# Kernel optimization log

Hardware: AMD Instinct MI355X
Metric: run time of the kernel (lower is better)

## Reference

```python
import jax, jax.numpy as jnp
import numpy as np


def setup_inputs() -> dict:
    key = jax.random.key(0)
    ks = jax.random.split(key, 4)
    B, H, W, C = 4, 64, 64, 256
    d = C // 8
    x = jax.random.normal(ks[0], (B, H, W, C), dtype=jnp.float32)
    wq = jax.random.normal(ks[1], (C, d), dtype=jnp.float32) * (1.0 / np.sqrt(C))
    wk = jax.random.normal(ks[2], (C, d), dtype=jnp.float32) * (1.0 / np.sqrt(C))
    wv = jax.random.normal(ks[3], (C, C), dtype=jnp.float32) * (1.0 / np.sqrt(C))
    bq = jnp.zeros((d,), dtype=jnp.float32)
    bk = jnp.zeros((d,), dtype=jnp.float32)
    bv = jnp.zeros((C,), dtype=jnp.float32)
    return {"x": x, "wq": wq, "bq": bq, "wk": wk, "bk": bk, "wv": wv, "bv": bv}


def reference(x, wq, bq, wk, bk, wv, bv):
    # x: [B, H, W, C] (channels-last, as in Keras Conv2D default)
    B, H, W, C = x.shape
    N = H * W
    xf = x.reshape(B, N, C)                      # 1x1 conv == per-pixel matmul
    q = xf @ wq + bq                             # [B, N, C//8]
    k = xf @ wk + bk                             # [B, N, C//8]
    v = xf @ wv + bv                             # [B, N, C]
    # NOTE: original module applies NO 1/sqrt(d) scaling.
    attn = jax.nn.softmax(jnp.einsum('bnd,bmd->bnm', q, k), axis=-1)  # [B, N, N]
    out = jnp.einsum('bnm,bmc->bnc', attn, v)    # [B, N, C]
    return out.reshape(B, H, W, C) + x
```

## Files before the change

### kernel.cpp

```cpp
#include <hip/hip_runtime.h>
#include <stdint.h>

typedef _Float16 f16;
typedef f16 half8 __attribute__((ext_vector_type(8)));
typedef f16 half4 __attribute__((ext_vector_type(4)));
typedef float floatx4 __attribute__((ext_vector_type(4)));

#define MFMA_F16(A, B, Cc) __builtin_amdgcn_mfma_f32_16x16x32_f16((A), (B), (Cc), 0, 0, 0)

static constexpr int NB  = 4;
static constexpr int NN  = 4096;
static constexpr int NC  = 256;
static constexpr int ND  = 32;
static constexpr int PIX = NB * NN;
static constexpr int NS  = 4;
static constexpr int KS  = NN / NS;

__device__ f16 g_WbT[320 * 256];
__device__ f16 g_Qh[(size_t)PIX * ND];
__device__ f16 g_Kh[(size_t)PIX * ND];
__device__ f16 g_VbT[(size_t)NB * NC * NN];
__device__ f16 g_Of[(size_t)NS * PIX * NC];
__device__ float g_m[NS * PIX];
__device__ float g_l[NS * PIX];

__device__ inline void gl2lds16(const f16* g, f16* l) {
  __builtin_amdgcn_global_load_lds(
      (const __attribute__((address_space(1))) void*)g,
      (__attribute__((address_space(3))) void*)l, 16, 0, 0);
}

__global__ __launch_bounds__(256) void prep_weights(const float* __restrict__ wq,
                                                    const float* __restrict__ wk,
                                                    const float* __restrict__ wv) {
  const int tid = blockIdx.x * 256 + threadIdx.x;
  if (tid >= 320 * 256) return;
  const int j = tid >> 8;
  const int k = tid & 255;
  float v;
  if (j < 32)      v = wq[k * 32 + j];
  else if (j < 64) v = wk[k * 32 + (j - 32)];
  else             v = wv[k * 256 + (j - 64)];
  g_WbT[j * 256 + k] = (f16)v;
}

__global__ __launch_bounds__(256) void proj_qkv(const float* __restrict__ x,
                                                const float* __restrict__ bq,
                                                const float* __restrict__ bk,
                                                const float* __restrict__ bv) {
  __shared__ f16 xs[64 * 32];
  __shared__ f16 wsT[320 * 32];
  __shared__ f16 vt[256 * 64];

  const int tid  = threadIdx.x;
  const int lane = tid & 63;
  const int wid  = tid >> 6;
  const int qd   = lane >> 4;
  const int c16  = lane & 15;
  const int p0   = blockIdx.x * 64;
  const floatx4 zero4 = {0.f, 0.f, 0.f, 0.f};

  floatx4 acc[20];
#pragma unroll
  for (int i = 0; i < 20; ++i) acc[i] = zero4;

  for (int kk = 0; kk < 256; kk += 32) {
    {
      const int r = tid >> 2, g = tid & 3;
      const floatx4* s4 = (const floatx4*)(x + (size_t)(p0 + r) * NC + kk + g * 8);
      const floatx4 xa = s4[0], xb = s4[1];
      half8 h;
      h[0] = (f16)xa[0]; h[1] = (f16)xa[1]; h[2] = (f16)xa[2]; h[3] = (f16)xa[3];
      h[4] = (f16)xb[0]; h[5] = (f16)xb[1]; h[6] = (f16)xb[2]; h[7] = (f16)xb[3];
      *(half8*)&xs[r * 32 + g * 8] = h;
    }
#pragma unroll
    for (int i = 0; i < 10; ++i) {
      const int cid = tid + 256 * i;
      const int j = cid >> 3, m = cid & 7;
      *(half4*)&wsT[j * 32 + m * 4] = *(const half4*)&g_WbT[j * 256 + kk + m * 4];
    }
    __syncthreads();
    const half8 a = *(const half8*)&xs[(wid * 16 + c16) * 32 + qd * 8];
#pragma unroll
    for (int nt = 0; nt < 20; ++nt) {
      const half8 bfr = *(const half8*)&wsT[(nt * 16 + c16) * 32 + qd * 8];
      acc[nt] = MFMA_F16(a, bfr, acc[nt]);
    }
    __syncthreads();
  }

#pragma unroll
  for (int nt = 0; nt < 20; ++nt) {
    const int j = nt * 16 + c16;
    const float bias = (j < 32) ? bq[j] : (j < 64) ? bk[j - 32] : bv[j - 64];
#pragma unroll
    for (int r = 0; r < 4; ++r) {
      const int rl = wid * 16 + qd * 4 + r;
      const int p  = p0 + rl;
      const float val = acc[nt][r] + bias;
      if (j < 32) {
        g_Qh[(size_t)p * ND + j] = (f16)(val * 1.44269504f);
      } else if (j < 64) {
        g_Kh[(size_t)p * ND + (j - 32)] = (f16)val;
      } else {
        vt[(j - 64) * 64 + rl] = (f16)val;
      }
    }
  }
  __syncthreads();
  const int b  = p0 >> 12;
  const int n0 = p0 & (NN - 1);
#pragma unroll
  for (int i = 0; i < 16; ++i) {
    const int cid = tid + 256 * i;
    const int c = cid >> 4, m = cid & 15;
    *(half4*)(g_VbT + ((size_t)(b * NC + c)) * NN + n0 + m * 4) =
        *(const half4*)&vt[c * 64 + m * 4];
  }
}

__global__ __launch_bounds__(256, 2) void attn_split(void) {
  __shared__ f16 vsT[256 * 64];
  __shared__ f16 ps[4][2][16 * 64];

  const int tid  = threadIdx.x;
  const int lane = tid & 63;
  const int wid  = tid >> 6;
  const int qd   = lane >> 4;
  const int c16  = lane & 15;
  const int b    = blockIdx.y;
  const int s    = blockIdx.z;
  const int q0   = blockIdx.x * 128 + wid * 32;
  const int sx7  = c16 & 7;
  const floatx4 zero4 = {0.f, 0.f, 0.f, 0.f};

  const int vrow = wid * 64 + (lane >> 3);
  const int vchk = (lane & 7) ^ ((lane >> 3) & 7);
  const f16* vlane = g_VbT + ((size_t)(b * NC + vrow)) * NN + vchk * 8;
  f16* vdst = &vsT[(size_t)wid * 4096 + (size_t)0];

  half8 qf[2];
#pragma unroll
  for (int g = 0; g < 2; ++g)
    qf[g] = *(const half8*)(g_Qh + ((size_t)(b * NN + q0 + g * 16 + c16)) * ND + qd * 8);

  floatx4 acc[2][16];
#pragma unroll
  for (int g = 0; g < 2; ++g)
#pragma unroll
    for (int i = 0; i < 16; ++i) acc[g][i] = zero4;
  float m_i[2] = {-1e30f, -1e30f};
  float l_p[2] = {0.f, 0.f};

  const int kbeg = s * KS, kend = (s + 1) * KS;

#pragma unroll
  for (int i = 0; i < 8; ++i)
    gl2lds16(vlane + kbeg + i * 8 * NN, vdst + i * 512);
  half8 kreg[4];
#pragma unroll
  for (int a = 0; a < 4; ++a)
    kreg[a] = *(const half8*)(g_Kh + ((size_t)(b * NN + kbeg + a * 16 + c16)) * ND + qd * 8);

  for (int k0 = kbeg; k0 < kend; k0 += 64) {
    floatx4 st[2][4];
#pragma unroll
    for (int g = 0; g < 2; ++g)
#pragma unroll
      for (int a = 0; a < 4; ++a) st[g][a] = MFMA_F16(kreg[a], qf[g], zero4);

    float tm[2];
#pragma unroll
    for (int g = 0; g < 2; ++g) {
      float t0 = fmaxf(fmaxf(st[g][0][0], st[g][0][1]), fmaxf(st[g][0][2], st[g][0][3]));
      float t1 = fmaxf(fmaxf(st[g][1][0], st[g][1][1]), fmaxf(st[g][1][2], st[g][1][3]));
      float t2 = fmaxf(fmaxf(st[g][2][0], st[g][2][1]), fmaxf(st[g][2][2], st[g][2][3]));
      float t3 = fmaxf(fmaxf(st[g][3][0], st[g][3][1]), fmaxf(st[g][3][2], st[g][3][3]));
      tm[g] = fmaxf(fmaxf(t0, t1), fmaxf(t2, t3));
    }
    if (__any(tm[0] > m_i[0] || tm[1] > m_i[1])) {
#pragma unroll
      for (int g = 0; g < 2; ++g) {
        float tr = tm[g];
        tr = fmaxf(tr, __shfl_xor(tr, 16));
        tr = fmaxf(tr, __shfl_xor(tr, 32));
        const float m_new = (tr > m_i[g]) ? tr + 5.0f : m_i[g];
        const float alpha = exp2f(m_i[g] - m_new);
        m_i[g] = m_new;
        l_p[g] *= alpha;
        float a4[4];
#pragma unroll
        for (int r = 0; r < 4; ++r) a4[r] = __shfl(alpha, qd * 4 + r);
#pragma unroll
        for (int ct = 0; ct < 16; ++ct)
#pragma unroll
          for (int r = 0; r < 4; ++r) acc[g][ct][r] *= a4[r];
      }
    }

#pragma unroll
    for (int g = 0; g < 2; ++g) {
      float ts = 0.f;
#pragma unroll
      for (int a = 0; a < 4; ++a) {
        half4 h;
#pragma unroll
        for (int r = 0; r < 4; ++r) {
          const float p = exp2f(st[g][a][r] - m_i[g]);
          ts += p;
          h[r] = (f16)p;
        }
        const int pc = ((a * 2 + (qd >> 1)) ^ sx7) * 8 + (qd & 1) * 4;
        *(half4*)&ps[wid][g][c16 * 64 + pc] = h;
      }
      l_p[g] += ts;
    }

    __syncthreads();

    const int k0n = (k0 + 64 < kend) ? (k0 + 64) : kbeg;
    half8 knew[4];
#pragma unroll
    for (int a = 0; a < 4; ++a)
      knew[a] = *(const half8*)(g_Kh + ((size_t)(b * NN + k0n + a * 16 + c16)) * ND + qd * 8);

    half8 pa[2][2];
#pragma unroll
    for (int g = 0; g < 2; ++g)
#pragma unroll
      for (int kh = 0; kh < 2; ++kh)
        pa[g][kh] = *(const half8*)&ps[wid][g][c16 * 64 + ((kh * 4 + qd) ^ sx7) * 8];
#pragma unroll
    for (int ct = 0; ct < 16; ++ct) {
#pragma unroll
      for (int kh = 0; kh < 2; ++kh) {
        const half8 bfr =
            *(const half8*)&vsT[(ct * 16 + c16) * 64 + ((kh * 4 + qd) ^ sx7) * 8];
        acc[0][ct] = MFMA_F16(pa[0][kh], bfr, acc[0][ct]);
        acc[1][ct] = MFMA_F16(pa[1][kh], bfr, acc[1][ct]);
      }
    }
    __syncthreads();

    if (k0 + 64 < kend) {
#pragma unroll
      for (int i = 0; i < 8; ++i)
        gl2lds16(vlane + (k0 + 64) + i * 8 * NN, vdst + i * 512);
    }
#pragma unroll
    for (int a = 0; a < 4; ++a) kreg[a] = knew[a];
  }

#pragma unroll
  for (int g = 0; g < 2; ++g) {
    float l = l_p[g];
    l += __shfl_xor(l, 16);
    l += __shfl_xor(l, 32);
    if (qd == 0) {
      const int row = b * NN + q0 + g * 16 + c16;
      g_m[s * PIX + row] = m_i[g];
      g_l[s * PIX + row] = l;
    }
    float linv[4];
#pragma unroll
    for (int r = 0; r < 4; ++r) linv[r] = 1.0f / __shfl(l, qd * 4 + r);
#pragma unroll
    for (int ct = 0; ct < 16; ++ct)
#pragma unroll
      for (int r = 0; r < 4; ++r) {
        const int qrow = q0 + g * 16 + qd * 4 + r;
        const int c = ct * 16 + c16;
        g_Of[((size_t)(s * PIX + b * NN + qrow)) * NC + c] = (f16)(acc[g][ct][r] * linv[r]);
      }
  }
}

__global__ __launch_bounds__(256) void combine(const float* __restrict__ x,
                                               float* __restrict__ out) {
  const int tid  = threadIdx.x;
  const int lane = tid & 63;
  const int wid  = tid >> 6;
  const int row  = blockIdx.x * 4 + wid;
  const int c    = lane * 4;

  float m[NS], l[NS], M = -1e30f;
#pragma unroll
  for (int s = 0; s < NS; ++s) {
    m[s] = g_m[s * PIX + row];
    l[s] = g_l[s * PIX + row];
    M = fmaxf(M, m[s]);
  }
  float w[NS], den = 0.f;
#pragma unroll
  for (int s = 0; s < NS; ++s) { w[s] = l[s] * exp2f(m[s] - M); den += w[s]; }
  const float inv = 1.0f / den;

  float a0 = 0.f, a1 = 0.f, a2 = 0.f, a3 = 0.f;
#pragma unroll
  for (int s = 0; s < NS; ++s) {
    const half4 h = *(const half4*)&g_Of[((size_t)(s * PIX + row)) * NC + c];
    const float ws = w[s] * inv;
    a0 += ws * (float)h[0];
    a1 += ws * (float)h[1];
    a2 += ws * (float)h[2];
    a3 += ws * (float)h[3];
  }
  const floatx4 xv = *(const floatx4*)&x[(size_t)row * NC + c];
  floatx4 o;
  o[0] = a0 + xv[0]; o[1] = a1 + xv[1]; o[2] = a2 + xv[2]; o[3] = a3 + xv[3];
  *(floatx4*)&out[(size_t)row * NC + c] = o;
}

extern "C" void kernel_launch(void* const* d_in, const int* in_sizes, int n_in,
                              void* d_out, int out_size, void* d_ws, size_t ws_size,
                              hipStream_t stream) {
  (void)in_sizes; (void)n_in; (void)d_ws; (void)ws_size; (void)out_size;
  const float* x  = (const float*)d_in[0];
  const float* wq = (const float*)d_in[1];
  const float* bq = (const float*)d_in[2];
  const float* wk = (const float*)d_in[3];
  const float* bk = (const float*)d_in[4];
  const float* wv = (const float*)d_in[5];
  const float* bv = (const float*)d_in[6];
  float* out = (float*)d_out;

  hipLaunchKernelGGL(prep_weights, dim3(320), dim3(256), 0, stream, wq, wk, wv);
  hipLaunchKernelGGL(proj_qkv, dim3(256), dim3(256), 0, stream, x, bq, bk, bv);
  hipLaunchKernelGGL(attn_split, dim3(NN / 128, NB, NS), dim3(256), 0, stream);
  hipLaunchKernelGGL(combine, dim3(PIX / 4), dim3(256), 0, stream, x, out);
}
```

Baseline: 164.9 us.

## Fuse split-K combine into attention kernel via last-block atomic counter

Removes the separate combine kernel. The last split block for each query tile, detected with an atomic counter and threadfences, merges the partial outputs and adds the residual. The residual now comes from an fp16 copy of x written during projection, which saves reading fp32 x but adds an extra global write and lowers residual precision. This saves one kernel launch and its tail. In exchange, the merge work is serialized in a few last-arriving blocks, which may extend the attention kernel's critical path.

```diff
diff --git a/kernel.cpp b/kernel.cpp
--- a/kernel.cpp
+++ b/kernel.cpp
@@ -15,14 +15,17 @@
 static constexpr int PIX = NB * NN;
 static constexpr int NS  = 4;
 static constexpr int KS  = NN / NS;
-
-__device__ f16 g_WbT[320 * 256];
-__device__ f16 g_Qh[(size_t)PIX * ND];
-__device__ f16 g_Kh[(size_t)PIX * ND];
-__device__ f16 g_VbT[(size_t)NB * NC * NN];
-__device__ f16 g_Of[(size_t)NS * PIX * NC];
+static constexpr int NT  = NB * (NN / 128);
+
+__device__ __align__(16) f16 g_Xh[(size_t)PIX * NC];
+__device__ __align__(16) f16 g_WbT[320 * 256];
+__device__ __align__(16) f16 g_Qh[(size_t)PIX * ND];
+__device__ __align__(16) f16 g_Kh[(size_t)PIX * ND];
+__device__ __align__(16) f16 g_VbT[(size_t)NB * NC * NN];
+__device__ __align__(16) f16 g_Of[(size_t)NS * PIX * NC];
 __device__ float g_m[NS * PIX];
 __device__ float g_l[NS * PIX];
+__device__ int   g_cnt[NT];
 
 __device__ inline void gl2lds16(const f16* g, f16* l) {
   __builtin_amdgcn_global_load_lds(
@@ -33,6 +36,7 @@
 __global__ __launch_bounds__(256) void prep_weights(const float* __restrict__ wq,
                                                     const float* __restrict__ wk,
                                                     const float* __restrict__ wv) {
+  if (blockIdx.x == 0 && threadIdx.x < NT) g_cnt[threadIdx.x] = 0;
   const int tid = blockIdx.x * 256 + threadIdx.x;
   if (tid >= 320 * 256) return;
   const int j = tid >> 8;
@@ -73,6 +77,7 @@
       h[0] = (f16)xa[0]; h[1] = (f16)xa[1]; h[2] = (f16)xa[2]; h[3] = (f16)xa[3];
       h[4] = (f16)xb[0]; h[5] = (f16)xb[1]; h[6] = (f16)xb[2]; h[7] = (f16)xb[3];
       *(half8*)&xs[r * 32 + g * 8] = h;
+      *(half8*)&g_Xh[(size_t)(p0 + r) * NC + kk + g * 8] = h;
     }
 #pragma unroll
     for (int i = 0; i < 10; ++i) {
@@ -120,9 +125,10 @@
   }
 }
 
-__global__ __launch_bounds__(256, 2) void attn_split(void) {
+__global__ __launch_bounds__(256, 2) void attn_split(float* __restrict__ out) {
   __shared__ f16 vsT[256 * 64];
   __shared__ f16 ps[4][2][16 * 64];
+  __shared__ int s_last;
 
   const int tid  = threadIdx.x;
   const int lane = tid & 63;
@@ -138,7 +144,7 @@
   const int vrow = wid * 64 + (lane >> 3);
   const int vchk = (lane & 7) ^ ((lane >> 3) & 7);
   const f16* vlane = g_VbT + ((size_t)(b * NC + vrow)) * NN + vchk * 8;
-  f16* vdst = &vsT[(size_t)wid * 4096 + (size_t)0];
+  f16* vdst = &vsT[(size_t)wid * 4096];
 
   half8 qf[2];
 #pragma unroll
@@ -274,42 +280,56 @@
         g_Of[((size_t)(s * PIX + b * NN + qrow)) * NC + c] = (f16)(acc[g][ct][r] * linv[r]);
       }
   }
-}
-
-__global__ __launch_bounds__(256) void combine(const float* __restrict__ x,
-                                               float* __restrict__ out) {
-  const int tid  = threadIdx.x;
-  const int lane = tid & 63;
-  const int wid  = tid >> 6;
-  const int row  = blockIdx.x * 4 + wid;
-  const int c    = lane * 4;
-
-  float m[NS], l[NS], M = -1e30f;
-#pragma unroll
-  for (int s = 0; s < NS; ++s) {
-    m[s] = g_m[s * PIX + row];
-    l[s] = g_l[s * PIX + row];
-    M = fmaxf(M, m[s]);
-  }
-  float w[NS], den = 0.f;
-#pragma unroll
-  for (int s = 0; s < NS; ++s) { w[s] = l[s] * exp2f(m[s] - M); den += w[s]; }
-  const float inv = 1.0f / den;
-
-  float a0 = 0.f, a1 = 0.f, a2 = 0.f, a3 = 0.f;
-#pragma unroll
-  for (int s = 0; s < NS; ++s) {
-    const half4 h = *(const half4*)&g_Of[((size_t)(s * PIX + row)) * NC + c];
-    const float ws = w[s] * inv;
-    a0 += ws * (float)h[0];
-    a1 += ws * (float)h[1];
-    a2 += ws * (float)h[2];
-    a3 += ws * (float)h[3];
-  }
-  const floatx4 xv = *(const floatx4*)&x[(size_t)row * NC + c];
-  floatx4 o;
-  o[0] = a0 + xv[0]; o[1] = a1 + xv[1]; o[2] = a2 + xv[2]; o[3] = a3 + xv[3];
-  *(floatx4*)&out[(size_t)row * NC + c] = o;
+
+  __threadfence();
+  __syncthreads();
+  if (tid == 0) s_last = (atomicAdd(&g_cnt[b * (NN / 128) + blockIdx.x], 1) == NS - 1);
+  __syncthreads();
+  if (!s_last) return;
+  __threadfence();
+
+  const int rowbase = b * NN + blockIdx.x * 128;
+  float* wbuf = (float*)ps;
+  if (tid < 128) {
+    const int row = rowbase + tid;
+    float mm[NS], ll[NS], M = -1e30f;
+#pragma unroll
+    for (int si = 0; si < NS; ++si) {
+      mm[si] = g_m[si * PIX + row];
+      ll[si] = g_l[si * PIX + row];
+      M = fmaxf(M, mm[si]);
+    }
+    float den = 0.f, w[NS];
+#pragma unroll
+    for (int si = 0; si < NS; ++si) { w[si] = ll[si] * exp2f(mm[si] - M); den += w[si]; }
+    const float inv = 1.0f / den;
+#pragma unroll
+    for (int si = 0; si < NS; ++si) wbuf[si * 128 + tid] = w[si] * inv;
+  }
+  __syncthreads();
+
+#pragma unroll
+  for (int rr = 0; rr < 16; ++rr) {
+    const int rl  = rr * 8 + (tid >> 5);
+    const int row = rowbase + rl;
+    const int ch  = (tid & 31) * 8;
+    float o[8] = {0.f, 0.f, 0.f, 0.f, 0.f, 0.f, 0.f, 0.f};
+#pragma unroll
+    for (int si = 0; si < NS; ++si) {
+      const half8 h = *(const half8*)&g_Of[((size_t)(si * PIX + row)) * NC + ch];
+      const float ws = wbuf[si * 128 + rl];
+#pragma unroll
+      for (int e = 0; e < 8; ++e) o[e] += ws * (float)h[e];
+    }
+    const half8 xv = *(const half8*)&g_Xh[(size_t)row * NC + ch];
+    floatx4 o0, o1;
+    o0[0] = o[0] + (float)xv[0]; o0[1] = o[1] + (float)xv[1];
+    o0[2] = o[2] + (float)xv[2]; o0[3] = o[3] + (float)xv[3];
+    o1[0] = o[4] + (float)xv[4]; o1[1] = o[5] + (float)xv[5];
+    o1[2] = o[6] + (float)xv[6]; o1[3] = o[7] + (float)xv[7];
+    *(floatx4*)&out[(size_t)row * NC + ch] = o0;
+    *(floatx4*)&out[(size_t)row * NC + ch + 4] = o1;
+  }
 }
 
 extern "C" void kernel_launch(void* const* d_in, const int* in_sizes, int n_in,
@@ -327,6 +347,5 @@
 
   hipLaunchKernelGGL(prep_weights, dim3(320), dim3(256), 0, stream, wq, wk, wv);
   hipLaunchKernelGGL(proj_qkv, dim3(256), dim3(256), 0, stream, x, bq, bk, bv);
-  hipLaunchKernelGGL(attn_split, dim3(NN / 128, NB, NS), dim3(256), 0, stream);
-  hipLaunchKernelGGL(combine, dim3(PIX / 4), dim3(256), 0, stream, x, out);
-}
+  hipLaunchKernelGGL(attn_split, dim3(NN / 128, NB, NS), dim3(256), 0, stream, out);
+}
```

After: 282.5 us. +71.4%, slower.

## Restructure QKV projection into smaller pixel tiles and read fp16 residual in combine

Applied to the files above, without the earlier changes.

The projection kernel now handles 32 pixels per block, staging the full fp16 row of x in padded shared memory once and looping over five 64-column weight chunks. This raises the block count and removes the repeated x conversion across k-steps. It also writes an fp16 copy of x that combine reads for the residual instead of fp32 x, cutting combine's read traffic. The trade-off is lower precision in the residual add and an extra global write of x in the projection.

```diff
diff --git a/kernel.cpp b/kernel.cpp
--- a/kernel.cpp
+++ b/kernel.cpp
@@ -16,11 +16,14 @@
 static constexpr int NS  = 4;
 static constexpr int KS  = NN / NS;
 
-__device__ f16 g_WbT[320 * 256];
-__device__ f16 g_Qh[(size_t)PIX * ND];
-__device__ f16 g_Kh[(size_t)PIX * ND];
-__device__ f16 g_VbT[(size_t)NB * NC * NN];
-__device__ f16 g_Of[(size_t)NS * PIX * NC];
+static constexpr int XP = 264;
+
+__device__ __align__(16) f16 g_Xh[(size_t)PIX * NC];
+__device__ __align__(16) f16 g_WbT[320 * 256];
+__device__ __align__(16) f16 g_Qh[(size_t)PIX * ND];
+__device__ __align__(16) f16 g_Kh[(size_t)PIX * ND];
+__device__ __align__(16) f16 g_VbT[(size_t)NB * NC * NN];
+__device__ __align__(16) f16 g_Of[(size_t)NS * PIX * NC];
 __device__ float g_m[NS * PIX];
 __device__ float g_l[NS * PIX];
 
@@ -48,75 +51,84 @@
                                                 const float* __restrict__ bq,
                                                 const float* __restrict__ bk,
                                                 const float* __restrict__ bv) {
-  __shared__ f16 xs[64 * 32];
-  __shared__ f16 wsT[320 * 32];
-  __shared__ f16 vt[256 * 64];
+  __shared__ f16 xs[32 * XP];
+  __shared__ f16 ws[64 * XP];
+  f16* vt = ws;
 
   const int tid  = threadIdx.x;
   const int lane = tid & 63;
   const int wid  = tid >> 6;
   const int qd   = lane >> 4;
   const int c16  = lane & 15;
-  const int p0   = blockIdx.x * 64;
+  const int p0   = blockIdx.x * 32;
+  const int b    = p0 >> 12;
+  const int n0   = p0 & (NN - 1);
   const floatx4 zero4 = {0.f, 0.f, 0.f, 0.f};
 
-  floatx4 acc[20];
-#pragma unroll
-  for (int i = 0; i < 20; ++i) acc[i] = zero4;
-
-  for (int kk = 0; kk < 256; kk += 32) {
+  {
+    const int r = tid >> 3, g = tid & 7;
+    const floatx4* src = (const floatx4*)(x + (size_t)(p0 + r) * NC + g * 32);
+#pragma unroll
+    for (int i = 0; i < 4; ++i) {
+      const floatx4 va = src[i * 2], vb = src[i * 2 + 1];
+      half8 h;
+      h[0] = (f16)va[0]; h[1] = (f16)va[1]; h[2] = (f16)va[2]; h[3] = (f16)va[3];
+      h[4] = (f16)vb[0]; h[5] = (f16)vb[1]; h[6] = (f16)vb[2]; h[7] = (f16)vb[3];
+      *(half8*)&xs[r * XP + g * 32 + i * 8] = h;
+      *(half8*)&g_Xh[(size_t)(p0 + r) * NC + g * 32 + i * 8] = h;
+    }
+  }
+
+  for (int ch = 0; ch < 5; ++ch) {
+    __syncthreads();
     {
-      const int r = tid >> 2, g = tid & 3;
-      const floatx4* s4 = (const floatx4*)(x + (size_t)(p0 + r) * NC + kk + g * 8);
-      const floatx4 xa = s4[0], xb = s4[1];
-      half8 h;
-      h[0] = (f16)xa[0]; h[1] = (f16)xa[1]; h[2] = (f16)xa[2]; h[3] = (f16)xa[3];
-      h[4] = (f16)xb[0]; h[5] = (f16)xb[1]; h[6] = (f16)xb[2]; h[7] = (f16)xb[3];
-      *(half8*)&xs[r * 32 + g * 8] = h;
-    }
-#pragma unroll
-    for (int i = 0; i < 10; ++i) {
-      const int cid = tid + 256 * i;
-      const int j = cid >> 3, m = cid & 7;
-      *(half4*)&wsT[j * 32 + m * 4] = *(const half4*)&g_WbT[j * 256 + kk + m * 4];
+      const int jj = tid >> 2, g = tid & 3;
+#pragma unroll
+      for (int i = 0; i < 8; ++i)
+        *(half8*)&ws[jj * XP + g * 64 + i * 8] =
+            *(const half8*)&g_WbT[(size_t)(ch * 64 + jj) * 256 + g * 64 + i * 8];
     }
     __syncthreads();
-    const half8 a = *(const half8*)&xs[(wid * 16 + c16) * 32 + qd * 8];
-#pragma unroll
-    for (int nt = 0; nt < 20; ++nt) {
-      const half8 bfr = *(const half8*)&wsT[(nt * 16 + c16) * 32 + qd * 8];
-      acc[nt] = MFMA_F16(a, bfr, acc[nt]);
-    }
-    __syncthreads();
-  }
-
-#pragma unroll
-  for (int nt = 0; nt < 20; ++nt) {
-    const int j = nt * 16 + c16;
-    const float bias = (j < 32) ? bq[j] : (j < 64) ? bk[j - 32] : bv[j - 64];
-#pragma unroll
-    for (int r = 0; r < 4; ++r) {
-      const int rl = wid * 16 + qd * 4 + r;
-      const int p  = p0 + rl;
-      const float val = acc[nt][r] + bias;
-      if (j < 32) {
-        g_Qh[(size_t)p * ND + j] = (f16)(val * 1.44269504f);
-      } else if (j < 64) {
-        g_Kh[(size_t)p * ND + (j - 32)] = (f16)val;
-      } else {
-        vt[(j - 64) * 64 + rl] = (f16)val;
-      }
-    }
-  }
-  __syncthreads();
-  const int b  = p0 >> 12;
-  const int n0 = p0 & (NN - 1);
-#pragma unroll
-  for (int i = 0; i < 16; ++i) {
-    const int cid = tid + 256 * i;
-    const int c = cid >> 4, m = cid & 15;
-    *(half4*)(g_VbT + ((size_t)(b * NC + c)) * NN + n0 + m * 4) =
-        *(const half4*)&vt[c * 64 + m * 4];
+
+    floatx4 acc2[2] = {zero4, zero4};
+    for (int kk = 0; kk < 256; kk += 32) {
+      const half8 bfr = *(const half8*)&ws[(wid * 16 + c16) * XP + kk + qd * 8];
+#pragma unroll
+      for (int rt = 0; rt < 2; ++rt) {
+        const half8 a = *(const half8*)&xs[(rt * 16 + c16) * XP + kk + qd * 8];
+        acc2[rt] = MFMA_F16(a, bfr, acc2[rt]);
+      }
+    }
+
+    if (ch == 0) {
+      const int j = wid * 16 + c16;
+      const float bias = (j < 32) ? bq[j] : bk[j - 32];
+#pragma unroll
+      for (int rt = 0; rt < 2; ++rt)
+#pragma unroll
+        for (int r = 0; r < 4; ++r) {
+          const int p = p0 + rt * 16 + qd * 4 + r;
+          const float val = acc2[rt][r] + bias;
+          if (j < 32) g_Qh[(size_t)p * ND + j] = (f16)(val * 1.44269504f);
+          else        g_Kh[(size_t)p * ND + (j - 32)] = (f16)val;
+        }
+    } else {
+      const int cl = wid * 16 + c16;
+      const float bias = bv[(ch - 1) * 64 + cl];
+      half4 h0, h1;
+#pragma unroll
+      for (int r = 0; r < 4; ++r) {
+        h0[r] = (f16)(acc2[0][r] + bias);
+        h1[r] = (f16)(acc2[1][r] + bias);
+      }
+      __syncthreads();
+      *(half4*)&vt[cl * 32 + qd * 4] = h0;
+      *(half4*)&vt[cl * 32 + 16 + qd * 4] = h1;
+      __syncthreads();
+      const int c = tid >> 2, part = tid & 3;
+      *(half8*)(g_VbT + ((size_t)(b * NC + (ch - 1) * 64 + c)) * NN + n0 + part * 8) =
+          *(const half8*)&vt[c * 32 + part * 8];
+    }
   }
 }
 
@@ -138,7 +150,7 @@
   const int vrow = wid * 64 + (lane >> 3);
   const int vchk = (lane & 7) ^ ((lane >> 3) & 7);
   const f16* vlane = g_VbT + ((size_t)(b * NC + vrow)) * NN + vchk * 8;
-  f16* vdst = &vsT[(size_t)wid * 4096 + (size_t)0];
+  f16* vdst = &vsT[(size_t)wid * 4096];
 
   half8 qf[2];
 #pragma unroll
@@ -276,8 +288,7 @@
   }
 }
 
-__global__ __launch_bounds__(256) void combine(const float* __restrict__ x,
-                                               float* __restrict__ out) {
+__global__ __launch_bounds__(256) void combine(float* __restrict__ out) {
   const int tid  = threadIdx.x;
   const int lane = tid & 63;
   const int wid  = tid >> 6;
@@ -306,9 +317,10 @@
     a2 += ws * (float)h[2];
     a3 += ws * (float)h[3];
   }
-  const floatx4 xv = *(const floatx4*)&x[(size_t)row * NC + c];
+  const half4 xv = *(const half4*)&g_Xh[(size_t)row * NC + c];
   floatx4 o;
-  o[0] = a0 + xv[0]; o[1] = a1 + xv[1]; o[2] = a2 + xv[2]; o[3] = a3 + xv[3];
+  o[0] = a0 + (float)xv[0]; o[1] = a1 + (float)xv[1];
+  o[2] = a2 + (float)xv[2]; o[3] = a3 + (float)xv[3];
   *(floatx4*)&out[(size_t)row * NC + c] = o;
 }
 
@@ -326,7 +338,7 @@
   float* out = (float*)d_out;
 
   hipLaunchKernelGGL(prep_weights, dim3(320), dim3(256), 0, stream, wq, wk, wv);
-  hipLaunchKernelGGL(proj_qkv, dim3(256), dim3(256), 0, stream, x, bq, bk, bv);
+  hipLaunchKernelGGL(proj_qkv, dim3(PIX / 32), dim3(256), 0, stream, x, bq, bk, bv);
   hipLaunchKernelGGL(attn_split, dim3(NN / 128, NB, NS), dim3(256), 0, stream);
-  hipLaunchKernelGGL(combine, dim3(PIX / 4), dim3(256), 0, stream, x, out);
-}
+  hipLaunchKernelGGL(combine, dim3(PIX / 4), dim3(256), 0, stream, out);
+}
```

Result: slower. 168.7 us (+2.4%).
